# Kernel tuning notes

Measured on AMD Instinct MI355X. Metric: run time of the kernel, lower is better.

The kernel has to match this reference:

```python
import jax, jax.numpy as jnp
import numpy as np
from jax import lax

NUM_LAYERS = 16
SPEED_OF_SOUND = 1500.0
DOMAIN_SIZE = 0.128
GRID_RES = 1024
KERNEL = 3
B, H, W = 8, 1024, 1024
DELTA_S = DOMAIN_SIZE / GRID_RES


def setup_inputs() -> dict:
    key = jax.random.key(0)
    k1, k2 = jax.random.split(key)
    T_init = jax.random.uniform(k1, (B, 1, H, W), dtype=jnp.float32)
    # speed-of-sound prediction kept strictly positive (avoid 1/0)
    sos_pred = jax.random.uniform(k2, (B, 1, H, W), dtype=jnp.float32) + 0.5
    # per-layer 3x3 conv kernels, filled with delta_s / c as in the torch init
    weights = jnp.full((NUM_LAYERS, 1, 1, KERNEL, KERNEL), DELTA_S / SPEED_OF_SOUND, dtype=jnp.float32)
    return {"T_init": T_init, "sos_pred": sos_pred, "weights": weights}


def reference(T_init, sos_pred, weights):
    # slowness is identical every iteration; compute once
    slowness = 1.0 / sos_pred  # [B,1,H,W]

    def step(T, w):
        # w: [1,1,3,3] (OIHW); SAME padding matches padding=kernel//2
        T_neighbors = lax.conv_general_dilated(
            T, w, window_strides=(1, 1), padding="SAME",
            dimension_numbers=("NCHW", "OIHW", "NCHW"))
        T = jnp.minimum(T, T_neighbors * slowness)
        return T, None

    T, _ = lax.scan(step, T_init, weights)
    return T
```

## Files before the change

kernel.cpp:

```cpp
#include <hip/hip_runtime.h>

#define HGT 1024
#define WID 1024
#define NB 8
#define NLAY 16

__global__ __launch_bounds__(256)
void eik_all(const float* __restrict__ Tin, const float* __restrict__ sos,
             const float* __restrict__ wts, float* __restrict__ Tout) {
    constexpr int TILE = 64, HALO = 16, P = 96;
    constexpr int LSTR = 99, LROWS = 98;
    constexpr int CW = 6, CH = 6;

    __shared__ float lds[LROWS * LSTR];
    __shared__ float swt[NLAY * 9];
    __shared__ float redT[4], redS[4];
    __shared__ unsigned redB[4];
    __shared__ unsigned decision;

    const int tid = threadIdx.x;

    const unsigned bphys = blockIdx.x;
    const unsigned Lt = (bphys & 7u) * 256u + (bphys >> 3u);
    const int bx = Lt & 15, by = (Lt >> 4) & 15, bz = Lt >> 8;
    const int gx0 = bx * TILE - HALO, gy0 = by * TILE - HALO;
    const size_t base = (size_t)bz * HGT * WID;

    if (tid < NLAY * 9) swt[tid] = wts[tid];

    float mT = 0.0f, mS = __builtin_huge_valf();
    unsigned bad = 0u;
    for (int i = tid; i < P * (P / 4); i += 256) {
        const int r = i / (P / 4), q = i % (P / 4);
        const int gy = gy0 + r, gx = gx0 + 4 * q;
        if (gy >= 0 && gy < HGT && gx >= 0 && gx < WID) {
            const size_t o = base + (size_t)gy * WID + gx;
            const float4 t = *reinterpret_cast<const float4*>(&Tin[o]);
            const float4 s = *reinterpret_cast<const float4*>(&sos[o]);
            bad |= (!(t.x >= 0.f)) | (!(t.y >= 0.f)) | (!(t.z >= 0.f)) | (!(t.w >= 0.f));
            bad |= (!(s.x >= 0.f)) | (!(s.y >= 0.f)) | (!(s.z >= 0.f)) | (!(s.w >= 0.f));
            mT = fmaxf(mT, fmaxf(fmaxf(t.x, t.y), fmaxf(t.z, t.w)));
            mS = fminf(mS, fminf(fminf(s.x, s.y), fminf(s.z, s.w)));
        }
    }
    #pragma unroll
    for (int off = 32; off > 0; off >>= 1) {
        mT = fmaxf(mT, __shfl_down(mT, off, 64));
        mS = fminf(mS, __shfl_down(mS, off, 64));
        bad |= __shfl_down(bad, off, 64);
    }
    const int wv = tid >> 6;
    if ((tid & 63) == 0) { redT[wv] = mT; redS[wv] = mS; redB[wv] = bad; }
    __syncthreads();
    if (tid == 0) {
        const float fT = fmaxf(fmaxf(redT[0], redT[1]), fmaxf(redT[2], redT[3]));
        const float fS = fminf(fminf(redS[0], redS[1]), fminf(redS[2], redS[3]));
        const unsigned fB = redB[0] | redB[1] | redB[2] | redB[3];
        unsigned dec = 0u;
        if (fB == 0u) {
            const float maxSlow = 1.0f / fS;
            float lb = log2f(fT);
            bool ok = true;
            #pragma unroll 1
            for (int l = 0; l < NLAY; ++l) {
                float ssum = 0.0f;
                #pragma unroll
                for (int k = 0; k < 9; ++k) {
                    const float w = swt[l * 9 + k];
                    ok &= (w >= 0.0f);
                    ssum += w;
                }
                lb += log2f(ssum * maxSlow);
            }
            if (ok && lb < -151.0f) dec = 1u;
        }
        decision = dec;
    }
    __syncthreads();

    if (decision != 0u) {
        #pragma unroll
        for (int k = 0; k < 4; ++k) {
            const int i = tid + k * 256;
            const int r = i >> 4, q = i & 15;
            *reinterpret_cast<float4*>(
                &Tout[base + (size_t)(gy0 + HALO + r) * WID + (gx0 + HALO + 4 * q)]) =
                make_float4(0.f, 0.f, 0.f, 0.f);
        }
        return;
    }

    for (int i = tid; i < LROWS * LSTR; i += 256) lds[i] = 0.0f;
    __syncthreads();
    for (int i = tid; i < P * P; i += 256) {
        const int r = i / P, c = i % P;
        const int gy = gy0 + r, gx = gx0 + c;
        float v = 0.0f;
        if (gy >= 0 && gy < HGT && gx >= 0 && gx < WID)
            v = Tin[base + (size_t)gy * WID + gx];
        lds[(r + 1) * LSTR + (c + 1)] = v;
    }

    const int tx = tid & 15, ty = tid >> 4;
    const int R0 = ty * CH, C0 = tx * CW;
    float slow[CH][CW];
    #pragma unroll
    for (int r = 0; r < CH; ++r) {
        #pragma unroll
        for (int j = 0; j < CW; ++j) {
            const int gy = gy0 + R0 + r, gx = gx0 + C0 + j;
            float sv = 1.0f;
            if (gy >= 0 && gy < HGT && gx >= 0 && gx < WID)
                sv = sos[base + (size_t)gy * WID + gx];
            slow[r][j] = 1.0f / sv;
        }
    }
    __syncthreads();

    float nw[CH][CW];
    #pragma unroll 1
    for (int it = 0; it < NLAY; ++it) {
        const float w00 = swt[it * 9 + 0], w01 = swt[it * 9 + 1], w02 = swt[it * 9 + 2];
        const float w10 = swt[it * 9 + 3], w11 = swt[it * 9 + 4], w12 = swt[it * 9 + 5];
        const float w20 = swt[it * 9 + 6], w21 = swt[it * 9 + 7], w22 = swt[it * 9 + 8];

        const bool uni = (w00 == w01) & (w01 == w02) & (w02 == w10) &
                         (w10 == w11) & (w11 == w12) & (w12 == w20) &
                         (w20 == w21) & (w21 == w22);

        float a[CW + 2], bb[CW + 2], cc[CW + 2];
        #pragma unroll
        for (int k = 0; k < CW + 2; ++k) a[k] = lds[R0 * LSTR + C0 + k];
        #pragma unroll
        for (int k = 0; k < CW + 2; ++k) bb[k] = lds[(R0 + 1) * LSTR + C0 + k];

        if (uni) {
            const float wu = w00;
            #pragma unroll
            for (int r = 0; r < CH; ++r) {
                #pragma unroll
                for (int k = 0; k < CW + 2; ++k) cc[k] = lds[(R0 + r + 2) * LSTR + C0 + k];
                float cs[CW + 2];
                #pragma unroll
                for (int k = 0; k < CW + 2; ++k) cs[k] = a[k] + bb[k] + cc[k];
                #pragma unroll
                for (int j = 0; j < CW; ++j) {
                    const float s9 = cs[j] + cs[j + 1] + cs[j + 2];
                    nw[r][j] = fminf(bb[j + 1], s9 * wu * slow[r][j]);
                }
                #pragma unroll
                for (int k = 0; k < CW + 2; ++k) { a[k] = bb[k]; bb[k] = cc[k]; }
            }
        } else {
            #pragma unroll
            for (int r = 0; r < CH; ++r) {
                #pragma unroll
                for (int k = 0; k < CW + 2; ++k) cc[k] = lds[(R0 + r + 2) * LSTR + C0 + k];
                #pragma unroll
                for (int j = 0; j < CW; ++j) {
                    float acc = a[j] * w00 + a[j + 1] * w01 + a[j + 2] * w02
                              + bb[j] * w10 + bb[j + 1] * w11 + bb[j + 2] * w12
                              + cc[j] * w20 + cc[j + 1] * w21 + cc[j + 2] * w22;
                    nw[r][j] = fminf(bb[j + 1], acc * slow[r][j]);
                }
                #pragma unroll
                for (int k = 0; k < CW + 2; ++k) { a[k] = bb[k]; bb[k] = cc[k]; }
            }
        }
        __syncthreads();
        #pragma unroll
        for (int r = 0; r < CH; ++r)
            #pragma unroll
            for (int j = 0; j < CW; ++j)
                lds[(R0 + r + 1) * LSTR + C0 + j + 1] = nw[r][j];
        __syncthreads();
    }

    #pragma unroll
    for (int k = 0; k < 4; ++k) {
        const int i = tid + k * 256;
        const int r = i >> 4, q = i & 15;
        const int o = (HALO + r + 1) * LSTR + HALO + 4 * q + 1;
        float4 v;
        v.x = lds[o]; v.y = lds[o + 1]; v.z = lds[o + 2]; v.w = lds[o + 3];
        *reinterpret_cast<float4*>(
            &Tout[base + (size_t)(gy0 + HALO + r) * WID + (gx0 + HALO + 4 * q)]) = v;
    }
}

extern "C" void kernel_launch(void* const* d_in, const int* in_sizes, int n_in,
                              void* d_out, int out_size, void* d_ws, size_t ws_size,
                              hipStream_t stream) {
    const float* T_init = (const float*)d_in[0];
    const float* sos    = (const float*)d_in[1];
    const float* wts    = (const float*)d_in[2];
    float* out = (float*)d_out;

    eik_all<<<dim3(2048), dim3(256), 0, stream>>>(T_init, sos, wts, out);
}
```

Before: 35.89 us.

## Hoist underflow-bound min/max check into a separate global reduction kernel

Adds a pre-pass kernel that reads T and sos once and writes one per-block partial of max T, min sos and a non-negativity flag into the workspace. The main kernel then combines these 1024 partials instead of re-reading its own 96x96 haloed tile of both inputs to decide whether every layer's result underflows to zero. This removes the halo-overlapped re-reads of the early-exit check, at the cost of an extra launch and each block reading 16 KB of partials. It also adds a fallback early exit that writes zeros when a block's loaded tile is entirely zero.

```diff
diff --git a/kernel.cpp b/kernel.cpp
--- a/kernel.cpp
+++ b/kernel.cpp
@@ -4,10 +4,48 @@
 #define WID 1024
 #define NB 8
 #define NLAY 16
+#define NPIX ((size_t)NB * HGT * WID)
+#define RBLKS 1024
+
+__global__ __launch_bounds__(256)
+void reduce_minmax(const float* __restrict__ T, const float* __restrict__ sos,
+                   uint4* __restrict__ partials) {
+    const float4* T4 = (const float4*)T;
+    const float4* S4 = (const float4*)sos;
+    float mT = 0.0f, mS = __builtin_huge_valf();
+    unsigned bad = 0u;
+    const size_t i0 = (size_t)blockIdx.x * 256 + threadIdx.x;
+    #pragma unroll
+    for (int k = 0; k < 8; ++k) {
+        const size_t i = i0 + (size_t)k * (RBLKS * 256);
+        const float4 t = T4[i], s = S4[i];
+        bad |= (!(t.x >= 0.f)) | (!(t.y >= 0.f)) | (!(t.z >= 0.f)) | (!(t.w >= 0.f));
+        bad |= (!(s.x >= 0.f)) | (!(s.y >= 0.f)) | (!(s.z >= 0.f)) | (!(s.w >= 0.f));
+        mT = fmaxf(mT, fmaxf(fmaxf(t.x, t.y), fmaxf(t.z, t.w)));
+        mS = fminf(mS, fminf(fminf(s.x, s.y), fminf(s.z, s.w)));
+    }
+    __shared__ float sT[256], sS[256];
+    __shared__ unsigned sB[256];
+    const int tid = threadIdx.x;
+    sT[tid] = mT; sS[tid] = mS; sB[tid] = bad;
+    __syncthreads();
+    for (int st = 128; st > 0; st >>= 1) {
+        if (tid < st) {
+            sT[tid] = fmaxf(sT[tid], sT[tid + st]);
+            sS[tid] = fminf(sS[tid], sS[tid + st]);
+            sB[tid] |= sB[tid + st];
+        }
+        __syncthreads();
+    }
+    if (tid == 0)
+        partials[blockIdx.x] =
+            make_uint4(__float_as_uint(sT[0]), __float_as_uint(sS[0]), sB[0], 0u);
+}
 
 __global__ __launch_bounds__(256)
 void eik_all(const float* __restrict__ Tin, const float* __restrict__ sos,
-             const float* __restrict__ wts, float* __restrict__ Tout) {
+             const float* __restrict__ wts, float* __restrict__ Tout,
+             const uint4* __restrict__ partials) {
     constexpr int TILE = 64, HALO = 16, P = 96;
     constexpr int LSTR = 99, LROWS = 98;
     constexpr int CW = 6, CH = 6;
@@ -30,17 +68,27 @@
 
     float mT = 0.0f, mS = __builtin_huge_valf();
     unsigned bad = 0u;
-    for (int i = tid; i < P * (P / 4); i += 256) {
-        const int r = i / (P / 4), q = i % (P / 4);
-        const int gy = gy0 + r, gx = gx0 + 4 * q;
-        if (gy >= 0 && gy < HGT && gx >= 0 && gx < WID) {
-            const size_t o = base + (size_t)gy * WID + gx;
-            const float4 t = *reinterpret_cast<const float4*>(&Tin[o]);
-            const float4 s = *reinterpret_cast<const float4*>(&sos[o]);
-            bad |= (!(t.x >= 0.f)) | (!(t.y >= 0.f)) | (!(t.z >= 0.f)) | (!(t.w >= 0.f));
-            bad |= (!(s.x >= 0.f)) | (!(s.y >= 0.f)) | (!(s.z >= 0.f)) | (!(s.w >= 0.f));
-            mT = fmaxf(mT, fmaxf(fmaxf(t.x, t.y), fmaxf(t.z, t.w)));
-            mS = fminf(mS, fminf(fminf(s.x, s.y), fminf(s.z, s.w)));
+    if (partials) {
+        #pragma unroll
+        for (int k = 0; k < RBLKS / 256; ++k) {
+            const uint4 p = partials[tid + k * 256];
+            mT = fmaxf(mT, __uint_as_float(p.x));
+            mS = fminf(mS, __uint_as_float(p.y));
+            bad |= p.z;
+        }
+    } else {
+        for (int i = tid; i < P * (P / 4); i += 256) {
+            const int r = i / (P / 4), q = i % (P / 4);
+            const int gy = gy0 + r, gx = gx0 + 4 * q;
+            if (gy >= 0 && gy < HGT && gx >= 0 && gx < WID) {
+                const size_t o = base + (size_t)gy * WID + gx;
+                const float4 t = *reinterpret_cast<const float4*>(&Tin[o]);
+                const float4 s = *reinterpret_cast<const float4*>(&sos[o]);
+                bad |= (!(t.x >= 0.f)) | (!(t.y >= 0.f)) | (!(t.z >= 0.f)) | (!(t.w >= 0.f));
+                bad |= (!(s.x >= 0.f)) | (!(s.y >= 0.f)) | (!(s.z >= 0.f)) | (!(s.w >= 0.f));
+                mT = fmaxf(mT, fmaxf(fmaxf(t.x, t.y), fmaxf(t.z, t.w)));
+                mS = fminf(mS, fminf(fminf(s.x, s.y), fminf(s.z, s.w)));
+            }
         }
     }
     #pragma unroll
@@ -92,13 +140,26 @@
 
     for (int i = tid; i < LROWS * LSTR; i += 256) lds[i] = 0.0f;
     __syncthreads();
+    unsigned nz = 0u;
     for (int i = tid; i < P * P; i += 256) {
         const int r = i / P, c = i % P;
         const int gy = gy0 + r, gx = gx0 + c;
         float v = 0.0f;
         if (gy >= 0 && gy < HGT && gx >= 0 && gx < WID)
             v = Tin[base + (size_t)gy * WID + gx];
+        nz |= __float_as_uint(v);
         lds[(r + 1) * LSTR + (c + 1)] = v;
+    }
+    if (__syncthreads_and(nz == 0u)) {
+        #pragma unroll
+        for (int k = 0; k < 4; ++k) {
+            const int i = tid + k * 256;
+            const int r = i >> 4, q = i & 15;
+            *reinterpret_cast<float4*>(
+                &Tout[base + (size_t)(gy0 + HALO + r) * WID + (gx0 + HALO + 4 * q)]) =
+                make_float4(0.f, 0.f, 0.f, 0.f);
+        }
+        return;
     }
 
     const int tx = tid & 15, ty = tid >> 4;
@@ -196,5 +257,9 @@
     const float* wts    = (const float*)d_in[2];
     float* out = (float*)d_out;
 
-    eik_all<<<dim3(2048), dim3(256), 0, stream>>>(T_init, sos, wts, out);
+    uint4* partials = (ws_size >= RBLKS * sizeof(uint4)) ? (uint4*)d_ws : nullptr;
+    if (partials)
+        reduce_minmax<<<dim3(RBLKS), dim3(256), 0, stream>>>(T_init, sos, partials);
+
+    eik_all<<<dim3(2048), dim3(256), 0, stream>>>(T_init, sos, wts, out, partials);
 }
```

Result: slower. 37.71 us (+5.1%).
